# Optimization experiments

Hardware: AMD Instinct MI355X
Metric: run time of the kernel (lower is better)

Reference implementation:

```python
import jax, jax.numpy as jnp
import numpy as np

B, O, D = 4096, 256, 256  # batch, size_out (rules), size_in (features)


def setup_inputs() -> dict:
    key = jax.random.key(0)
    k1, k2, k3, k4, k5 = jax.random.split(key, 5)
    return {
        "x": jax.random.normal(k1, (B, D), dtype=jnp.float32),
        "scales": jax.random.normal(k2, (O, D), dtype=jnp.float32),
        # strict upper triangle holds the packed rot vectors (original inits them to zeros;
        # small values keep the quadratic form well conditioned)
        "rots": jax.random.normal(k3, (O, D, D), dtype=jnp.float32) * 0.02,
        "centroids": jax.random.normal(k4, (O, D, 1), dtype=jnp.float32),
        "b": jax.random.uniform(k5, (O,), dtype=jnp.float32, minval=0.5, maxval=1.5),
    }


def reference(x, scales, rots, centroids, b):
    # Build symmetric transform A[o] = diag(scales[o]) + triu(rots[o],1) + triu(rots[o],1)^T
    # (equivalent to the loop of diag_embed(r_i, i+1) + mirrored lower diagonal).
    upper = jnp.triu(rots, 1)                                   # [O,D,D]
    A = upper + jnp.swapaxes(upper, -1, -2)
    A = A + jnp.eye(D, dtype=scales.dtype) * scales[:, None, :]  # diag_embed(scales)
    # Augmented affine map: mul[o,i,b'] = A[o] @ x[b'] + centroid[o,i]; const row dropped
    # since only the first size_in rows feed the norm.
    y = jnp.einsum('bj,oij->boi', x, A) + centroids[..., 0][None, :, :]  # [B,O,D]
    rx = jnp.sqrt(jnp.sum(y * y, axis=-1))                      # L2 norm over D -> [B,O]
    return 1.0 / (1.0 + rx ** (2.0 * b))                        # bell membership [B,O]
```

## Files before the change

### kernel.cpp

```cpp
#include <hip/hip_runtime.h>
#include <cstdint>
#include <cmath>

#define Bn 4096
#define Dn 256
#define On 256

typedef __bf16 v8bf __attribute__((ext_vector_type(8)));
typedef float  v4f  __attribute__((ext_vector_type(4)));
typedef unsigned short us8 __attribute__((ext_vector_type(8)));

__device__ __forceinline__ unsigned short f2bf(float f) {
    unsigned int u = __builtin_bit_cast(unsigned int, f);
    unsigned int r = (u + 0x7fffu + ((u >> 16) & 1u)) >> 16;
    return (unsigned short)r;
}

__device__ __forceinline__ void gl_lds16(const void* g, void* l) {
    __builtin_amdgcn_global_load_lds(
        (const __attribute__((address_space(1))) void*)(uintptr_t)g,
        (__attribute__((address_space(3))) void*)(uintptr_t)l, 16, 0, 0);
}

__global__ __launch_bounds__(256) void prep_x(const float* __restrict__ x,
                                              unsigned short* __restrict__ xb) {
    const int tid = threadIdx.x;
    const int cb  = blockIdx.x;
#pragma unroll
    for (int s = 0; s < 4; ++s) {
        const int i = cb * 4096 + s * 1024 + tid * 4;
        const float4 v = *(const float4*)(x + i);
        ushort4 u;
        u.x = f2bf(v.x); u.y = f2bf(v.y); u.z = f2bf(v.z); u.w = f2bf(v.w);
        *(ushort4*)(xb + i) = u;
    }
}

template <int TIv, int TJv>
__device__ __forceinline__ void extract_pair(const float* T, v8bf (&af)[4][8],
                                             const float (&sc4)[4],
                                             int wv, int frow, int quad) {
    if (TIv == TJv) {
        if (wv == TIv) {
#pragma unroll
            for (int mi = 0; mi < 4; ++mi) {
                const int r = mi * 16 + frow;
#pragma unroll
                for (int kl = 0; kl < 2; ++kl) {
                    us8 u;
#pragma unroll
                    for (int q = 0; q < 8; ++q) {
                        const int cc = kl * 32 + quad * 8 + q;
                        const float v = (r < cc) ? T[r * 64 + cc]
                                      : ((r > cc) ? T[cc * 64 + r] : sc4[mi]);
                        u[q] = f2bf(v);
                    }
                    af[mi][TJv * 2 + kl] = __builtin_bit_cast(v8bf, u);
                }
            }
        }
    } else {
        if (wv == TIv) {
#pragma unroll
            for (int mi = 0; mi < 4; ++mi) {
                const int r = mi * 16 + frow;
#pragma unroll
                for (int kl = 0; kl < 2; ++kl) {
                    const float4 a = *(const float4*)&T[r * 64 + kl * 32 + quad * 8];
                    const float4 b = *(const float4*)&T[r * 64 + kl * 32 + quad * 8 + 4];
                    us8 u;
                    u[0] = f2bf(a.x); u[1] = f2bf(a.y); u[2] = f2bf(a.z); u[3] = f2bf(a.w);
                    u[4] = f2bf(b.x); u[5] = f2bf(b.y); u[6] = f2bf(b.z); u[7] = f2bf(b.w);
                    af[mi][TJv * 2 + kl] = __builtin_bit_cast(v8bf, u);
                }
            }
        } else if (wv == TJv) {
#pragma unroll
            for (int mi = 0; mi < 4; ++mi) {
                const int c = mi * 16 + frow;
#pragma unroll
                for (int kl = 0; kl < 2; ++kl) {
                    us8 u;
#pragma unroll
                    for (int q = 0; q < 8; ++q)
                        u[q] = f2bf(T[(kl * 32 + quad * 8 + q) * 64 + c]);
                    af[mi][TIv * 2 + kl] = __builtin_bit_cast(v8bf, u);
                }
            }
        }
    }
}

#define WAITV(N)                                         \
    do {                                                 \
        asm volatile("s_waitcnt vmcnt(" #N ")" ::: "memory"); \
        __builtin_amdgcn_sched_barrier(0);               \
    } while (0)
#define LGKM0()                                          \
    do {                                                 \
        asm volatile("s_waitcnt lgkmcnt(0)" ::: "memory"); \
        __builtin_amdgcn_sched_barrier(0);               \
    } while (0)
#define BARF()                                           \
    do {                                                 \
        __builtin_amdgcn_sched_barrier(0);               \
        __builtin_amdgcn_s_barrier();                    \
        __builtin_amdgcn_sched_barrier(0);               \
    } while (0)

#define STAGE_T(TIv, TJv, SLOT)                                              \
    do {                                                                     \
        const float* s_ = rbase + (TIv) * (64 * Dn) + (TJv) * 64;            \
        float* d_ = tileB + (SLOT) * 4096;                                   \
        _Pragma("unroll")                                                    \
        for (int s = 0; s < 4; ++s) {                                        \
            const int idx = s * 256 + tid;                                   \
            gl_lds16(s_ + (idx >> 4) * Dn + (idx & 15) * 4, d_ + idx * 4);   \
        }                                                                    \
    } while (0)

__global__ __launch_bounds__(256, 2) void fuzzy_main(
    const float* __restrict__ rots, const float* __restrict__ scales,
    const unsigned short* __restrict__ xb, const float* __restrict__ cent,
    const float* __restrict__ bvals, float* __restrict__ out) {
    __shared__ __align__(16) unsigned short Xs[2][4][64 * 64];
    __shared__ float ssbuf[2][4][64];

    const int tid  = threadIdx.x;
    const int lane = tid & 63;
    const int wv   = tid >> 6;
    const int Lb = blockIdx.x;
    const int o     = (Lb & 7) * 32 + ((Lb >> 3) & 31);
    const int bhalf = Lb >> 8;

    const int frow = lane & 15, quad = lane >> 4, f3 = lane & 7;
    const int lr = lane >> 3, ls = lane & 7;
    const int ksw = (ls ^ lr) * 8;

    float cv[4][4];
#pragma unroll
    for (int mi = 0; mi < 4; ++mi)
#pragma unroll
        for (int rg = 0; rg < 4; ++rg)
            cv[mi][rg] = cent[o * Dn + wv * 64 + mi * 16 + quad * 4 + rg];

    float sc4[4];
#pragma unroll
    for (int mi = 0; mi < 4; ++mi)
        sc4[mi] = scales[o * Dn + wv * 64 + mi * 16 + frow];

    float* const tileB = (float*)&Xs[0][0][0];
    const float* const rbase = rots + ((size_t)o << 16);

    v8bf af[4][8];

    STAGE_T(0, 0, 0); STAGE_T(0, 1, 1); STAGE_T(0, 2, 2);

    WAITV(8); BARF(); extract_pair<0, 0>(tileB + 0,    af, sc4, wv, frow, quad); LGKM0(); BARF(); STAGE_T(0, 3, 0);
    WAITV(8); BARF(); extract_pair<0, 1>(tileB + 4096, af, sc4, wv, frow, quad); LGKM0(); BARF(); STAGE_T(1, 1, 1);
    WAITV(8); BARF(); extract_pair<0, 2>(tileB + 8192, af, sc4, wv, frow, quad); LGKM0(); BARF(); STAGE_T(1, 2, 2);
    WAITV(8); BARF(); extract_pair<0, 3>(tileB + 0,    af, sc4, wv, frow, quad); LGKM0(); BARF(); STAGE_T(1, 3, 0);
    WAITV(8); BARF(); extract_pair<1, 1>(tileB + 4096, af, sc4, wv, frow, quad); LGKM0(); BARF(); STAGE_T(2, 2, 1);
    WAITV(8); BARF(); extract_pair<1, 2>(tileB + 8192, af, sc4, wv, frow, quad); LGKM0(); BARF(); STAGE_T(2, 3, 2);
    WAITV(8); BARF(); extract_pair<1, 3>(tileB + 0,    af, sc4, wv, frow, quad); LGKM0(); BARF(); STAGE_T(3, 3, 0);
    WAITV(8); BARF(); extract_pair<2, 2>(tileB + 4096, af, sc4, wv, frow, quad); LGKM0(); BARF();
    WAITV(4); BARF(); extract_pair<2, 3>(tileB + 8192, af, sc4, wv, frow, quad); LGKM0(); BARF();
    WAITV(0); BARF(); extract_pair<3, 3>(tileB + 0,    af, sc4, wv, frow, quad); LGKM0(); BARF();

    {
        const int b0 = bhalf * 2048;
#pragma unroll
        for (int c = 0; c < 4; ++c)
#pragma unroll
            for (int q = 0; q < 2; ++q) {
                const int row = (wv * 2 + q) * 8 + lr;
                gl_lds16(xb + (size_t)(b0 + row) * Dn + c * 64 + ksw,
                         &Xs[0][c][row * 64 + ls * 8]);
            }
    }
    __syncthreads();

    for (int it = 0; it < 32; ++it) {
        const int buf = it & 1;
        const int b0  = bhalf * 2048 + it * 64;
        if (it < 31) {
            const int nb0 = b0 + 64;
#pragma unroll
            for (int c = 0; c < 4; ++c)
#pragma unroll
                for (int q = 0; q < 2; ++q) {
                    const int row = (wv * 2 + q) * 8 + lr;
                    gl_lds16(xb + (size_t)(nb0 + row) * Dn + c * 64 + ksw,
                             &Xs[buf ^ 1][c][row * 64 + ls * 8]);
                }
        }

        v4f acc[4][4];
#pragma unroll
        for (int mi = 0; mi < 4; ++mi)
#pragma unroll
            for (int ni = 0; ni < 4; ++ni)
                acc[mi][ni] = v4f{0.f, 0.f, 0.f, 0.f};

#pragma unroll
        for (int t = 0; t < 8; ++t) {
            v8bf xf[4];
            const int sl = ((t & 1) * 4 + quad) ^ f3;
#pragma unroll
            for (int ni = 0; ni < 4; ++ni)
                xf[ni] = *(const v8bf*)&Xs[buf][t >> 1][(ni * 16 + frow) * 64 + sl * 8];
#pragma unroll
            for (int mi = 0; mi < 4; ++mi)
#pragma unroll
                for (int ni = 0; ni < 4; ++ni)
                    acc[mi][ni] = __builtin_amdgcn_mfma_f32_16x16x32_bf16(
                        af[mi][t], xf[ni], acc[mi][ni], 0, 0, 0);
        }

#pragma unroll
        for (int ni = 0; ni < 4; ++ni) {
            float v = 0.f;
#pragma unroll
            for (int mi = 0; mi < 4; ++mi)
#pragma unroll
                for (int rg = 0; rg < 4; ++rg) {
                    const float y = acc[mi][ni][rg] + cv[mi][rg];
                    v += y * y;
                }
            v += __shfl_xor(v, 16);
            v += __shfl_xor(v, 32);
            if (lane < 16) ssbuf[buf][wv][ni * 16 + lane] = v;
        }
        __syncthreads();
        if (tid < 64) {
            const float ssq = ssbuf[buf][0][tid] + ssbuf[buf][1][tid] +
                              ssbuf[buf][2][tid] + ssbuf[buf][3][tid];
            out[(size_t)(b0 + tid) * On + o] = 1.0f / (1.0f + powf(ssq, bvals[o]));
        }
    }
}

__global__ void fallback_kernel(const float* __restrict__ x, const float* __restrict__ scales,
                                const float* __restrict__ rots, const float* __restrict__ cent,
                                const float* __restrict__ bvals, float* __restrict__ out) {
    const int b = blockIdx.x * blockDim.x + threadIdx.x;
    const int o = blockIdx.y;
    if (b >= Bn) return;
    const float* R  = rots + (size_t)o * Dn * Dn;
    const float* xv = x + (size_t)b * Dn;
    float ss = 0.f;
    for (int i = 0; i < Dn; ++i) {
        float a = cent[o * Dn + i];
        for (int j = 0; j < Dn; ++j) {
            const float w = (j > i) ? R[i * Dn + j]
                          : ((j < i) ? R[j * Dn + i] : scales[o * Dn + i]);
            a += w * xv[j];
        }
        ss += a * a;
    }
    out[(size_t)b * On + o] = 1.f / (1.f + powf(ss, bvals[o]));
}

extern "C" void kernel_launch(void* const* d_in, const int* in_sizes, int n_in,
                              void* d_out, int out_size, void* d_ws, size_t ws_size,
                              hipStream_t stream) {
    const float* x         = (const float*)d_in[0];
    const float* scales    = (const float*)d_in[1];
    const float* rots      = (const float*)d_in[2];
    const float* centroids = (const float*)d_in[3];
    const float* bvals     = (const float*)d_in[4];
    float* out = (float*)d_out;

    const size_t needX = (size_t)Bn * Dn * sizeof(unsigned short);

    if (ws_size >= needX) {
        unsigned short* xb = (unsigned short*)d_ws;
        prep_x<<<dim3(256), 256, 0, stream>>>(x, xb);
        fuzzy_main<<<dim3(512), 256, 0, stream>>>(rots, scales, xb, centroids, bvals, out);
    } else {
        fallback_kernel<<<dim3(Bn / 256, On), 256, 0, stream>>>(x, scales, rots, centroids,
                                                                bvals, out);
    }
}
```

Measured before the change: 227.3 us.

## Switch to 32x32x16 MFMA with k-major x layout and swizzled rot staging

Replaces the 16x16x32 MFMA tiles with 32x32x16 bf16 MFMAs, and transposes x in the prep kernel into a k-chunk-major bf16 layout so each lane's B fragment is one contiguous 16-byte LDS read. Rot tiles are staged with an XOR swizzle and paired, two tiles per stage, so the prologue runs in fewer barrier rounds. The membership write for each batch tile is deferred to the next iteration so it overlaps the next compute, and powf is replaced by exp2/log2. Intent is fewer MFMA issues and LDS reads per FLOP and less prologue synchronisation, at the cost of larger accumulator register use and a more complex layout.

```diff
diff --git a/kernel.cpp b/kernel.cpp
--- a/kernel.cpp
+++ b/kernel.cpp
@@ -7,7 +7,7 @@
 #define On 256
 
 typedef __bf16 v8bf __attribute__((ext_vector_type(8)));
-typedef float  v4f  __attribute__((ext_vector_type(4)));
+typedef float  v16f __attribute__((ext_vector_type(16)));
 typedef unsigned short us8 __attribute__((ext_vector_type(8)));
 
 __device__ __forceinline__ unsigned short f2bf(float f) {
@@ -23,220 +23,250 @@
 }
 
 __global__ __launch_bounds__(256) void prep_x(const float* __restrict__ x,
-                                              unsigned short* __restrict__ xb) {
+                                              unsigned short* __restrict__ xbT) {
+    __shared__ float t[64][68];
     const int tid = threadIdx.x;
-    const int cb  = blockIdx.x;
+    const int bb = blockIdx.x >> 2;
+    const int kb = blockIdx.x & 3;
+    const int b0 = bb * 64;
 #pragma unroll
     for (int s = 0; s < 4; ++s) {
-        const int i = cb * 4096 + s * 1024 + tid * 4;
-        const float4 v = *(const float4*)(x + i);
-        ushort4 u;
-        u.x = f2bf(v.x); u.y = f2bf(v.y); u.z = f2bf(v.z); u.w = f2bf(v.w);
-        *(ushort4*)(xb + i) = u;
-    }
-}
-
-template <int TIv, int TJv>
-__device__ __forceinline__ void extract_pair(const float* T, v8bf (&af)[4][8],
-                                             const float (&sc4)[4],
-                                             int wv, int frow, int quad) {
-    if (TIv == TJv) {
-        if (wv == TIv) {
-#pragma unroll
-            for (int mi = 0; mi < 4; ++mi) {
-                const int r = mi * 16 + frow;
-#pragma unroll
-                for (int kl = 0; kl < 2; ++kl) {
+        const int idx = s * 256 + tid;
+        const int r = idx >> 4, c4 = idx & 15;
+        const float4 v = *(const float4*)(x + (size_t)(b0 + r) * Dn + kb * 64 + c4 * 4);
+        *(float4*)&t[r][c4 * 4] = v;
+    }
+    __syncthreads();
+    const int lane = tid & 63, wv = tid >> 6;
+#pragma unroll
+    for (int s = 0; s < 2; ++s) {
+        const int kcl = s * 4 + wv;
+        us8 u;
+#pragma unroll
+        for (int q = 0; q < 8; ++q) u[q] = f2bf(t[lane][kcl * 8 + q]);
+        *(us8*)(xbT + ((size_t)(kb * 8 + kcl) * Bn + b0 + lane) * 8) = u;
+    }
+}
+
+template <int TI, int TJ>
+__device__ __forceinline__ void extract_pair(const float* T, v8bf (&af)[2][16],
+                                             const float (&sc2)[2],
+                                             int wv, int lane) {
+    const int l31 = lane & 31, hw = lane >> 5;
+    if (TI == TJ) {
+        if (wv == TI) {
+#pragma unroll
+            for (int mt = 0; mt < 2; ++mt) {
+                const int r = mt * 32 + l31;
+                const int mr = (r & 7) << 2;
+#pragma unroll
+                for (int kq = 0; kq < 4; ++kq) {
                     us8 u;
 #pragma unroll
                     for (int q = 0; q < 8; ++q) {
-                        const int cc = kl * 32 + quad * 8 + q;
-                        const float v = (r < cc) ? T[r * 64 + cc]
-                                      : ((r > cc) ? T[cc * 64 + r] : sc4[mi]);
+                        const int c = kq * 16 + hw * 8 + q;
+                        const float v = (r < c) ? T[r * 64 + (c ^ mr)]
+                                      : ((r > c) ? T[c * 64 + (r ^ ((c & 7) << 2))]
+                                                 : sc2[mt]);
                         u[q] = f2bf(v);
                     }
-                    af[mi][TJv * 2 + kl] = __builtin_bit_cast(v8bf, u);
+                    af[mt][TJ * 4 + kq] = __builtin_bit_cast(v8bf, u);
                 }
             }
         }
     } else {
-        if (wv == TIv) {
-#pragma unroll
-            for (int mi = 0; mi < 4; ++mi) {
-                const int r = mi * 16 + frow;
-#pragma unroll
-                for (int kl = 0; kl < 2; ++kl) {
-                    const float4 a = *(const float4*)&T[r * 64 + kl * 32 + quad * 8];
-                    const float4 b = *(const float4*)&T[r * 64 + kl * 32 + quad * 8 + 4];
+        if (wv == TI) {
+#pragma unroll
+            for (int mt = 0; mt < 2; ++mt) {
+                const int r = mt * 32 + l31;
+                const int mr = (r & 7) << 2;
+#pragma unroll
+                for (int kq = 0; kq < 4; ++kq) {
+                    const int c0 = kq * 16 + hw * 8;
+                    const float4 a = *(const float4*)&T[r * 64 + (c0 ^ mr)];
+                    const float4 b = *(const float4*)&T[r * 64 + ((c0 + 4) ^ mr)];
                     us8 u;
                     u[0] = f2bf(a.x); u[1] = f2bf(a.y); u[2] = f2bf(a.z); u[3] = f2bf(a.w);
                     u[4] = f2bf(b.x); u[5] = f2bf(b.y); u[6] = f2bf(b.z); u[7] = f2bf(b.w);
-                    af[mi][TJv * 2 + kl] = __builtin_bit_cast(v8bf, u);
+                    af[mt][TJ * 4 + kq] = __builtin_bit_cast(v8bf, u);
                 }
             }
-        } else if (wv == TJv) {
-#pragma unroll
-            for (int mi = 0; mi < 4; ++mi) {
-                const int c = mi * 16 + frow;
-#pragma unroll
-                for (int kl = 0; kl < 2; ++kl) {
+        } else if (wv == TJ) {
+#pragma unroll
+            for (int mt = 0; mt < 2; ++mt) {
+                const int cL = mt * 32 + l31;
+#pragma unroll
+                for (int kq = 0; kq < 4; ++kq) {
                     us8 u;
 #pragma unroll
-                    for (int q = 0; q < 8; ++q)
-                        u[q] = f2bf(T[(kl * 32 + quad * 8 + q) * 64 + c]);
-                    af[mi][TIv * 2 + kl] = __builtin_bit_cast(v8bf, u);
+                    for (int q = 0; q < 8; ++q) {
+                        const int rL = kq * 16 + hw * 8 + q;
+                        u[q] = f2bf(T[rL * 64 + (cL ^ ((rL & 7) << 2))]);
+                    }
+                    af[mt][TI * 4 + kq] = __builtin_bit_cast(v8bf, u);
                 }
             }
         }
     }
 }
 
-#define WAITV(N)                                         \
-    do {                                                 \
+#define WAITV(N)                                              \
+    do {                                                      \
         asm volatile("s_waitcnt vmcnt(" #N ")" ::: "memory"); \
-        __builtin_amdgcn_sched_barrier(0);               \
-    } while (0)
-#define LGKM0()                                          \
-    do {                                                 \
-        asm volatile("s_waitcnt lgkmcnt(0)" ::: "memory"); \
-        __builtin_amdgcn_sched_barrier(0);               \
-    } while (0)
-#define BARF()                                           \
-    do {                                                 \
-        __builtin_amdgcn_sched_barrier(0);               \
-        __builtin_amdgcn_s_barrier();                    \
-        __builtin_amdgcn_sched_barrier(0);               \
-    } while (0)
-
-#define STAGE_T(TIv, TJv, SLOT)                                              \
+        __builtin_amdgcn_sched_barrier(0);                    \
+    } while (0)
+#define LGKM0()                                               \
+    do {                                                      \
+        asm volatile("s_waitcnt lgkmcnt(0)" ::: "memory");    \
+        __builtin_amdgcn_sched_barrier(0);                    \
+    } while (0)
+#define BARF()                                                \
+    do {                                                      \
+        __builtin_amdgcn_sched_barrier(0);                    \
+        __builtin_amdgcn_s_barrier();                         \
+        __builtin_amdgcn_sched_barrier(0);                    \
+    } while (0)
+
+#define STAGE_T(TIv, TJv, DST)                                               \
     do {                                                                     \
         const float* s_ = rbase + (TIv) * (64 * Dn) + (TJv) * 64;            \
-        float* d_ = tileB + (SLOT) * 4096;                                   \
         _Pragma("unroll")                                                    \
         for (int s = 0; s < 4; ++s) {                                        \
             const int idx = s * 256 + tid;                                   \
-            gl_lds16(s_ + (idx >> 4) * Dn + (idx & 15) * 4, d_ + idx * 4);   \
+            const int r = idx >> 4, c4 = idx & 15;                           \
+            gl_lds16(s_ + (size_t)r * Dn + ((c4 ^ (r & 7)) * 4),             \
+                     (DST) + idx * 4);                                       \
+        }                                                                    \
+    } while (0)
+
+#define XSTAGE(BUF, B0)                                                      \
+    do {                                                                     \
+        _Pragma("unroll")                                                    \
+        for (int s = 0; s < 8; ++s) {                                        \
+            gl_lds16(xbT + ((size_t)(s * 4 + wv) * Bn + (B0) + lane) * 8,    \
+                     &Xs[BUF][s * 256 + tid][0]);                            \
         }                                                                    \
     } while (0)
 
 __global__ __launch_bounds__(256, 2) void fuzzy_main(
     const float* __restrict__ rots, const float* __restrict__ scales,
-    const unsigned short* __restrict__ xb, const float* __restrict__ cent,
+    const unsigned short* __restrict__ xbT, const float* __restrict__ cent,
     const float* __restrict__ bvals, float* __restrict__ out) {
-    __shared__ __align__(16) unsigned short Xs[2][4][64 * 64];
+    __shared__ __align__(16) unsigned short Xs[2][2048][8];
     __shared__ float ssbuf[2][4][64];
+    __shared__ float centL[Dn];
 
     const int tid  = threadIdx.x;
     const int lane = tid & 63;
     const int wv   = tid >> 6;
+    const int l31  = lane & 31, hw = lane >> 5;
     const int Lb = blockIdx.x;
     const int o     = (Lb & 7) * 32 + ((Lb >> 3) & 31);
     const int bhalf = Lb >> 8;
 
-    const int frow = lane & 15, quad = lane >> 4, f3 = lane & 7;
-    const int lr = lane >> 3, ls = lane & 7;
-    const int ksw = (ls ^ lr) * 8;
-
-    float cv[4][4];
-#pragma unroll
-    for (int mi = 0; mi < 4; ++mi)
-#pragma unroll
-        for (int rg = 0; rg < 4; ++rg)
-            cv[mi][rg] = cent[o * Dn + wv * 64 + mi * 16 + quad * 4 + rg];
-
-    float sc4[4];
-#pragma unroll
-    for (int mi = 0; mi < 4; ++mi)
-        sc4[mi] = scales[o * Dn + wv * 64 + mi * 16 + frow];
-
-    float* const tileB = (float*)&Xs[0][0][0];
+    centL[tid] = cent[o * Dn + tid];
+    float sc2[2];
+#pragma unroll
+    for (int mt = 0; mt < 2; ++mt)
+        sc2[mt] = scales[o * Dn + wv * 64 + mt * 32 + l31];
+    const float bv = bvals[o];
+
+    WAITV(0);
+
+    float* const S0 = (float*)&Xs[1][0][0];
+    float* const S1 = S0 + 4096;
+    float* const S2 = (float*)&Xs[0][0][0];
+    float* const S3 = S2 + 4096;
     const float* const rbase = rots + ((size_t)o << 16);
 
-    v8bf af[4][8];
-
-    STAGE_T(0, 0, 0); STAGE_T(0, 1, 1); STAGE_T(0, 2, 2);
-
-    WAITV(8); BARF(); extract_pair<0, 0>(tileB + 0,    af, sc4, wv, frow, quad); LGKM0(); BARF(); STAGE_T(0, 3, 0);
-    WAITV(8); BARF(); extract_pair<0, 1>(tileB + 4096, af, sc4, wv, frow, quad); LGKM0(); BARF(); STAGE_T(1, 1, 1);
-    WAITV(8); BARF(); extract_pair<0, 2>(tileB + 8192, af, sc4, wv, frow, quad); LGKM0(); BARF(); STAGE_T(1, 2, 2);
-    WAITV(8); BARF(); extract_pair<0, 3>(tileB + 0,    af, sc4, wv, frow, quad); LGKM0(); BARF(); STAGE_T(1, 3, 0);
-    WAITV(8); BARF(); extract_pair<1, 1>(tileB + 4096, af, sc4, wv, frow, quad); LGKM0(); BARF(); STAGE_T(2, 2, 1);
-    WAITV(8); BARF(); extract_pair<1, 2>(tileB + 8192, af, sc4, wv, frow, quad); LGKM0(); BARF(); STAGE_T(2, 3, 2);
-    WAITV(8); BARF(); extract_pair<1, 3>(tileB + 0,    af, sc4, wv, frow, quad); LGKM0(); BARF(); STAGE_T(3, 3, 0);
-    WAITV(8); BARF(); extract_pair<2, 2>(tileB + 4096, af, sc4, wv, frow, quad); LGKM0(); BARF();
-    WAITV(4); BARF(); extract_pair<2, 3>(tileB + 8192, af, sc4, wv, frow, quad); LGKM0(); BARF();
-    WAITV(0); BARF(); extract_pair<3, 3>(tileB + 0,    af, sc4, wv, frow, quad); LGKM0(); BARF();
-
-    {
-        const int b0 = bhalf * 2048;
-#pragma unroll
-        for (int c = 0; c < 4; ++c)
-#pragma unroll
-            for (int q = 0; q < 2; ++q) {
-                const int row = (wv * 2 + q) * 8 + lr;
-                gl_lds16(xb + (size_t)(b0 + row) * Dn + c * 64 + ksw,
-                         &Xs[0][c][row * 64 + ls * 8]);
-            }
-    }
+    v8bf af[2][16];
+
+    STAGE_T(0, 1, S0); STAGE_T(2, 3, S1);
+    STAGE_T(0, 2, S2); STAGE_T(1, 3, S3);
+    WAITV(8); BARF();
+    extract_pair<0, 1>(S0, af, sc2, wv, lane);
+    extract_pair<2, 3>(S1, af, sc2, wv, lane);
+    LGKM0(); BARF();
+    STAGE_T(0, 3, S0); STAGE_T(1, 2, S1);
+    WAITV(8); BARF();
+    extract_pair<0, 2>(S2, af, sc2, wv, lane);
+    extract_pair<1, 3>(S3, af, sc2, wv, lane);
+    LGKM0(); BARF();
+    STAGE_T(0, 0, S2); STAGE_T(1, 1, S3);
+    WAITV(8); BARF();
+    extract_pair<0, 3>(S0, af, sc2, wv, lane);
+    extract_pair<1, 2>(S1, af, sc2, wv, lane);
+    LGKM0(); BARF();
+    STAGE_T(2, 2, S0); STAGE_T(3, 3, S1);
+    WAITV(8); BARF();
+    extract_pair<0, 0>(S2, af, sc2, wv, lane);
+    extract_pair<1, 1>(S3, af, sc2, wv, lane);
+    LGKM0(); BARF();
+    WAITV(0); BARF();
+    extract_pair<2, 2>(S0, af, sc2, wv, lane);
+    extract_pair<3, 3>(S1, af, sc2, wv, lane);
+    LGKM0(); BARF();
+
+    XSTAGE(0, bhalf * 2048);
     __syncthreads();
 
     for (int it = 0; it < 32; ++it) {
         const int buf = it & 1;
         const int b0  = bhalf * 2048 + it * 64;
-        if (it < 31) {
-            const int nb0 = b0 + 64;
-#pragma unroll
-            for (int c = 0; c < 4; ++c)
-#pragma unroll
-                for (int q = 0; q < 2; ++q) {
-                    const int row = (wv * 2 + q) * 8 + lr;
-                    gl_lds16(xb + (size_t)(nb0 + row) * Dn + c * 64 + ksw,
-                             &Xs[buf ^ 1][c][row * 64 + ls * 8]);
-                }
-        }
-
-        v4f acc[4][4];
-#pragma unroll
-        for (int mi = 0; mi < 4; ++mi)
-#pragma unroll
-            for (int ni = 0; ni < 4; ++ni)
-                acc[mi][ni] = v4f{0.f, 0.f, 0.f, 0.f};
-
-#pragma unroll
-        for (int t = 0; t < 8; ++t) {
-            v8bf xf[4];
-            const int sl = ((t & 1) * 4 + quad) ^ f3;
-#pragma unroll
-            for (int ni = 0; ni < 4; ++ni)
-                xf[ni] = *(const v8bf*)&Xs[buf][t >> 1][(ni * 16 + frow) * 64 + sl * 8];
-#pragma unroll
-            for (int mi = 0; mi < 4; ++mi)
-#pragma unroll
-                for (int ni = 0; ni < 4; ++ni)
-                    acc[mi][ni] = __builtin_amdgcn_mfma_f32_16x16x32_bf16(
-                        af[mi][t], xf[ni], acc[mi][ni], 0, 0, 0);
-        }
-
-#pragma unroll
-        for (int ni = 0; ni < 4; ++ni) {
+        if (it < 31) XSTAGE(buf ^ 1, b0 + 64);
+
+        if (it > 0 && lane < 16) {
+            const int bl = wv * 16 + lane;
+            const float ssq = ssbuf[buf ^ 1][0][bl] + ssbuf[buf ^ 1][1][bl] +
+                              ssbuf[buf ^ 1][2][bl] + ssbuf[buf ^ 1][3][bl];
+            out[(size_t)(b0 - 64 + bl) * On + o] =
+                1.0f / (1.0f + exp2f(bv * log2f(ssq)));
+        }
+
+        v16f acc[2][2];
+#pragma unroll
+        for (int mt = 0; mt < 2; ++mt)
+#pragma unroll
+            for (int nt = 0; nt < 2; ++nt)
+#pragma unroll
+                for (int rg = 0; rg < 16; ++rg) acc[mt][nt][rg] = 0.f;
+
+#pragma unroll
+        for (int ks = 0; ks < 16; ++ks) {
+            v8bf xf[2];
+#pragma unroll
+            for (int nt = 0; nt < 2; ++nt)
+                xf[nt] = *(const v8bf*)&Xs[buf][(ks * 2 + hw) * 64 + nt * 32 + l31][0];
+#pragma unroll
+            for (int mt = 0; mt < 2; ++mt)
+#pragma unroll
+                for (int nt = 0; nt < 2; ++nt)
+                    acc[mt][nt] = __builtin_amdgcn_mfma_f32_32x32x16_bf16(
+                        af[mt][ks], xf[nt], acc[mt][nt], 0, 0, 0);
+        }
+
+#pragma unroll
+        for (int nt = 0; nt < 2; ++nt) {
             float v = 0.f;
 #pragma unroll
-            for (int mi = 0; mi < 4; ++mi)
-#pragma unroll
-                for (int rg = 0; rg < 4; ++rg) {
-                    const float y = acc[mi][ni][rg] + cv[mi][rg];
+            for (int mt = 0; mt < 2; ++mt)
+#pragma unroll
+                for (int rg = 0; rg < 16; ++rg) {
+                    const float y = acc[mt][nt][rg] +
+                        centL[wv * 64 + mt * 32 + (rg & 3) + 8 * (rg >> 2) + 4 * hw];
                     v += y * y;
                 }
-            v += __shfl_xor(v, 16);
             v += __shfl_xor(v, 32);
-            if (lane < 16) ssbuf[buf][wv][ni * 16 + lane] = v;
+            if (lane < 32) ssbuf[buf][wv][nt * 32 + lane] = v;
         }
         __syncthreads();
-        if (tid < 64) {
-            const float ssq = ssbuf[buf][0][tid] + ssbuf[buf][1][tid] +
-                              ssbuf[buf][2][tid] + ssbuf[buf][3][tid];
-            out[(size_t)(b0 + tid) * On + o] = 1.0f / (1.0f + powf(ssq, bvals[o]));
-        }
+    }
+    if (lane < 16) {
+        const int bl = wv * 16 + lane;
+        const float ssq = ssbuf[1][0][bl] + ssbuf[1][1][bl] +
+                          ssbuf[1][2][bl] + ssbuf[1][3][bl];
+        out[(size_t)(bhalf * 2048 + 31 * 64 + bl) * On + o] =
+            1.0f / (1.0f + exp2f(bv * log2f(ssq)));
     }
 }
 
@@ -274,9 +304,9 @@
     const size_t needX = (size_t)Bn * Dn * sizeof(unsigned short);
 
     if (ws_size >= needX) {
-        unsigned short* xb = (unsigned short*)d_ws;
-        prep_x<<<dim3(256), 256, 0, stream>>>(x, xb);
-        fuzzy_main<<<dim3(512), 256, 0, stream>>>(rots, scales, xb, centroids, bvals, out);
+        unsigned short* xbT = (unsigned short*)d_ws;
+        prep_x<<<dim3(256), 256, 0, stream>>>(x, xbT);
+        fuzzy_main<<<dim3(512), 256, 0, stream>>>(rots, scales, xbT, centroids, bvals, out);
     } else {
         fallback_kernel<<<dim3(Bn / 256, On), 256, 0, stream>>>(x, scales, rots, centroids,
                                                                 bvals, out);
```

Result: no change. 225.9 us (-0.6%).
